# Optimization experiments

Hardware: AMD Instinct MI355X
Metric: run time of the kernel (lower is better)

Reference implementation:

```python
import jax, jax.numpy as jnp
import numpy as np

B, S, D, C, H, E, K, L = 32, 512, 768, 3072, 1024, 8, 2, 2


def _layernorm(x, g, b, eps=1e-5):
    mu = jnp.mean(x, axis=-1, keepdims=True)
    var = jnp.var(x, axis=-1, keepdims=True)
    return (x - mu) * jax.lax.rsqrt(var + eps) * g + b


def setup_inputs() -> dict:
    key = jax.random.key(0)
    ks = jax.random.split(key, 12)
    s = 0.02
    return {
        "hidden_states": jax.random.normal(ks[0], (B, S, C), jnp.float32),
        "proj_w": jax.random.normal(ks[1], (C, D), jnp.float32) * s,
        "proj_b": jnp.zeros((D,), jnp.float32),
        "ln1_g": jnp.ones((D,), jnp.float32),
        "ln1_b": jnp.zeros((D,), jnp.float32),
        "gate_w": jax.random.normal(ks[2], (D, E), jnp.float32) * s,
        "gate_b": jnp.zeros((E,), jnp.float32),
        "w1": jax.random.normal(ks[3], (E, D, H), jnp.float32) * s,
        "b1": jnp.zeros((E, H), jnp.float32),
        "w2": jax.random.normal(ks[4], (E, H, D), jnp.float32) * s,
        "b2": jnp.zeros((E, D), jnp.float32),
        "ln2_g": jnp.ones((D,), jnp.float32),
        "ln2_b": jnp.zeros((D,), jnp.float32),
        "cls_w": jax.random.normal(ks[5], (D, L), jnp.float32) * s,
        "cls_b": jnp.zeros((L,), jnp.float32),
    }


def reference(hidden_states, proj_w, proj_b, ln1_g, ln1_b, gate_w, gate_b,
              w1, b1, w2, b2, ln2_g, ln2_b, cls_w, cls_b):
    # layer_projection: Linear -> LayerNorm -> GELU (dropout = identity in eval)
    x = jnp.einsum('bsc,cd->bsd', hidden_states, proj_w) + proj_b
    x = _layernorm(x, ln1_g, ln1_b)
    seq_out = jax.nn.gelu(x, approximate=False)  # [B,S,D]

    # Router: gate -> softmax -> top-k -> renormalize
    probs = jax.nn.softmax(seq_out @ gate_w + gate_b, axis=-1)  # [B,S,E]
    top_w, top_i = jax.lax.top_k(probs, K)                      # [B,S,K]
    top_w = top_w / jnp.sum(top_w, axis=-1, keepdims=True)

    # combine[t,e] = sum_k top_w[t,k] * (top_i[t,k]==e)
    combine = jnp.sum(jax.nn.one_hot(top_i, E, dtype=top_w.dtype)
                      * top_w[..., None], axis=-2)              # [B,S,E]

    xt = seq_out.reshape(-1, D)                                 # [T,D]
    ct = combine.reshape(-1, E)                                 # [T,E]
    h = jax.nn.gelu(jnp.einsum('td,edh->eth', xt, w1) + b1[:, None, :],
                    approximate=False)                          # [E,T,H]
    eo = jnp.einsum('eth,ehd->etd', h, w2) + b2[:, None, :]     # [E,T,D]
    moe = jnp.einsum('etd,te->td', eo, ct).reshape(B, S, D)

    moe = _layernorm(moe + seq_out, ln2_g, ln2_b)
    logits = moe @ cls_w + cls_b                                # [B,S,2]
    return logits
```

## Files before the change

### kernel.cpp

```cpp
#include <hip/hip_runtime.h>
#include <hip/hip_bf16.h>

#define T_TOK 16384
#define CDIM 3072
#define DDIM 768
#define HDIM 1024
#define NEXP 8
#define NSLOT 33792
#define MAXTILE 264
#define AMB_CAP 2048
#define AMB2_CAP 256
#define KSPLIT 4
#define NSEG 8

typedef __attribute__((ext_vector_type(8))) short bfrag;
typedef __attribute__((ext_vector_type(4))) float f32x4;
typedef __attribute__((ext_vector_type(4))) float fvec4;

__device__ __forceinline__ unsigned short bf16_rn(float f) {
  union { float f; unsigned u; } v; v.f = f;
  unsigned r = v.u + 0x7fffu + ((v.u >> 16) & 1u);
  return (unsigned short)(r >> 16);
}
__device__ __forceinline__ float bf16_f32(unsigned short h) {
  union { unsigned u; float f; } v; v.u = ((unsigned)h) << 16;
  return v.f;
}
__device__ __forceinline__ float gelu_exact(float x) {
  return 0.5f * x * (1.0f + erff(x * 0.70710678118654752440f));
}
__device__ __forceinline__ void glds16(const void* g, void* l) {
  __builtin_amdgcn_global_load_lds((const __attribute__((address_space(1))) void*)g,
                                   (__attribute__((address_space(3))) void*)l, 16, 0, 0);
}

__global__ void k_init(int* token_list, int* counts, int* cursors, unsigned short* zero_row,
                       int* amb_count, int* amb2_count) {
  int i = blockIdx.x * 256 + threadIdx.x;
  for (int j = i; j < NSLOT; j += 64 * 256) token_list[j] = -1;
  if (i < NEXP) counts[i] = 0;
  if (i < 128) cursors[i] = 0;
  if (i == 0) { *amb_count = 0; *amb2_count = 0; }
  if (i < 1024) zero_row[i] = 0;
}

__global__ void k_cast_tiled(const float* __restrict__ src,
                             unsigned short* __restrict__ dst) {
  __shared__ unsigned short h[128][136];
  int rb = blockIdx.x;
  int cc = blockIdx.y;
  int tid = threadIdx.x;
  const float* in = src + ((size_t)rb * 128) * CDIM + cc * 128;
#pragma unroll
  for (int it = 0; it < 16; ++it) {
    int idx = it * 256 + tid;
    int r = idx >> 5, nv = idx & 31;
    fvec4 v = *(const fvec4*)(in + (size_t)r * CDIM + nv * 4);
    unsigned long long p = (unsigned long long)bf16_rn(v[0]) |
                           ((unsigned long long)bf16_rn(v[1]) << 16) |
                           ((unsigned long long)bf16_rn(v[2]) << 32) |
                           ((unsigned long long)bf16_rn(v[3]) << 48);
    *(unsigned long long*)&h[r][nv * 4] = p;
  }
  __syncthreads();
  unsigned short* ob = dst + ((size_t)rb * 96 + cc * 4) * 4096;
#pragma unroll
  for (int kt = 0; kt < 4; ++kt) {
#pragma unroll
    for (int it = 0; it < 2; ++it) {
      int gg = it * 256 + tid;
      int kg = gg >> 7, r = gg & 127;
      bfrag o = *(const bfrag*)&h[r][kt * 32 + kg * 8];
      *(bfrag*)(ob + ((size_t)kt * 512 + gg) * 8) = o;
    }
  }
}

__global__ void k_transpose_split(const float* __restrict__ src,
                                  unsigned short* __restrict__ dhi,
                                  unsigned short* __restrict__ dlo) {
  __shared__ unsigned short h[128][72], l[128][72];
  int nb2 = blockIdx.x;
  int cb = blockIdx.y;
  int col_blk = nb2 >> 1, nhalf = nb2 & 1;
  int n0 = col_blk * 128 + nhalf * 64;
  int tid = threadIdx.x;
  const float* in = src + (size_t)(cb * 128) * DDIM + n0;
#pragma unroll
  for (int it = 0; it < 8; ++it) {
    int idx = it * 256 + tid;
    int cl = idx >> 4, nv = idx & 15;
    fvec4 v = *(const fvec4*)(in + (size_t)cl * DDIM + nv * 4);
    unsigned long long ph = 0, pl = 0;
#pragma unroll
    for (int e = 0; e < 4; ++e) {
      unsigned short hh = bf16_rn(v[e]);
      unsigned short ll = bf16_rn(v[e] - bf16_f32(hh));
      ph |= (unsigned long long)hh << (16 * e);
      pl |= (unsigned long long)ll << (16 * e);
    }
    *(unsigned long long*)&h[cl][nv * 4] = ph;
    *(unsigned long long*)&l[cl][nv * 4] = pl;
  }
  __syncthreads();
  size_t obase = ((size_t)col_blk * 96 + cb * 4) * 4096;
#pragma unroll
  for (int kt = 0; kt < 4; ++kt) {
    int kg = tid >> 6, rl = tid & 63;
    bfrag oh, ol;
#pragma unroll
    for (int e = 0; e < 8; ++e) {
      int c = kt * 32 + kg * 8 + e;
      oh[e] = (short)h[c][rl];
      ol[e] = (short)l[c][rl];
    }
    size_t gi = obase + ((size_t)kt * 512 + kg * 128 + nhalf * 64 + rl) * 8;
    *(bfrag*)(dhi + gi) = oh;
    *(bfrag*)(dlo + gi) = ol;
  }
}

__global__ void k_transpose_tiled(const float* __restrict__ src0,
                                  unsigned short* __restrict__ dst0, int K, int N) {
  __shared__ unsigned short h[128][72];
  int nb2 = blockIdx.x;
  int cb = blockIdx.y;
  int z = blockIdx.z;
  int col_blk = nb2 >> 1, nhalf = nb2 & 1;
  int n0 = col_blk * 128 + nhalf * 64;
  int tid = threadIdx.x;
  const float* in = src0 + (size_t)z * K * N + (size_t)(cb * 128) * N + n0;
#pragma unroll
  for (int it = 0; it < 8; ++it) {
    int idx = it * 256 + tid;
    int cl = idx >> 4, nv = idx & 15;
    fvec4 v = *(const fvec4*)(in + (size_t)cl * N + nv * 4);
    unsigned long long ph = 0;
#pragma unroll
    for (int e = 0; e < 4; ++e)
      ph |= (unsigned long long)bf16_rn(v[e]) << (16 * e);
    *(unsigned long long*)&h[cl][nv * 4] = ph;
  }
  __syncthreads();
  size_t obase = (size_t)z * K * N + ((size_t)col_blk * (K / 32) + cb * 4) * 4096;
#pragma unroll
  for (int kt = 0; kt < 4; ++kt) {
    int kg = tid >> 6, rl = tid & 63;
    bfrag oh;
#pragma unroll
    for (int e = 0; e < 8; ++e) oh[e] = (short)h[kt * 32 + kg * 8 + e][rl];
    *(bfrag*)(dst0 + obase + ((size_t)kt * 512 + kg * 128 + nhalf * 64 + rl) * 8) = oh;
  }
}

__launch_bounds__(256, 3)
__global__ void k_gemm1(const unsigned short* __restrict__ Atil,
                        const unsigned short* __restrict__ Btil,
                        float* __restrict__ Cout)
{
  __shared__ unsigned short sA[12288], sB[12288];
  int tid = threadIdx.x;
  int lane = tid & 63, wave = tid >> 6;
  int id = blockIdx.x;
  int swz = (id & 7) * 96 + (id >> 3);
  int brow = swz / 6, bcol = swz % 6;
  int row0 = brow * 128, col0 = bcol * 128;
  int wm = wave >> 1, wn = wave & 1;

  f32x4 acc[4][4];
#pragma unroll
  for (int i = 0; i < 4; ++i)
#pragma unroll
    for (int j = 0; j < 4; ++j) acc[i][j] = (f32x4){0.f, 0.f, 0.f, 0.f};

  int rsel = lane & 15, kq = lane >> 4;
  const unsigned short* At = Atil + (size_t)(brow * 96) * 4096;
  const unsigned short* Bt = Btil + (size_t)(bcol * 96) * 4096;

  auto STAGE = [&](int kt, int b) {
    const unsigned short* as = At + (size_t)kt * 4096;
    const unsigned short* bs = Bt + (size_t)kt * 4096;
    int lbase = b * 4096;
#pragma unroll
    for (int pass = 0; pass < 2; ++pass) {
      int g = pass * 256 + tid;
      int li = lbase + (pass * 256 + wave * 64) * 8;
      glds16(as + (size_t)g * 8, &sA[li]);
      glds16(bs + (size_t)g * 8, &sB[li]);
    }
  };

  STAGE(0, 0);
  STAGE(1, 1);
  int b0 = 0;
  for (int kt = 0; kt < 96; ++kt) {
    if (kt < 95) asm volatile("s_waitcnt vmcnt(4)" ::: "memory");
    else         asm volatile("s_waitcnt vmcnt(0)" ::: "memory");
    __builtin_amdgcn_s_barrier();
    if (kt + 2 < 96) {
      int bn = b0 + 2; if (bn >= 3) bn -= 3;
      STAGE(kt + 2, bn);
    }
    int lb = b0 * 4096;
    bfrag af[4], bf[4];
#pragma unroll
    for (int i = 0; i < 4; ++i) {
      af[i] = *(const bfrag*)&sA[lb + (kq * 128 + wm * 64 + i * 16 + rsel) * 8];
      bf[i] = *(const bfrag*)&sB[lb + (kq * 128 + wn * 64 + i * 16 + rsel) * 8];
    }
#pragma unroll
    for (int i = 0; i < 4; ++i)
#pragma unroll
      for (int j = 0; j < 4; ++j)
        acc[i][j] = __builtin_amdgcn_mfma_f32_16x16x32_bf16(af[i], bf[j], acc[i][j], 0, 0, 0);
    b0 = (b0 == 2) ? 0 : b0 + 1;
  }

  int cc = lane & 15, rr = (lane >> 4) * 4;
#pragma unroll
  for (int i = 0; i < 4; ++i)
#pragma unroll
    for (int j = 0; j < 4; ++j)
#pragma unroll
      for (int r = 0; r < 4; ++r) {
        int row = row0 + wm * 64 + i * 16 + rr + r;
        int col = col0 + wn * 64 + j * 16 + cc;
        Cout[(size_t)row * DDIM + col] = acc[i][j][r];
      }
}

__launch_bounds__(256)
__global__ void k_ln_router(const float* __restrict__ xw, const float* __restrict__ proj_b,
                            const float* __restrict__ g1, const float* __restrict__ b1v,
                            const float* __restrict__ gate_w, const float* __restrict__ gate_b,
                            unsigned short* __restrict__ seq_b16,
                            int* __restrict__ top_i, float* __restrict__ top_w,
                            int* __restrict__ amb_list, int* __restrict__ amb_count)
{
  int lane = threadIdx.x & 63;
  int t = blockIdx.x * 4 + (threadIdx.x >> 6);
  const float* xr = xw + (size_t)t * DDIM;
  float x0[12];
  float s = 0.f, s2 = 0.f;
#pragma unroll
  for (int j = 0; j < 12; ++j) {
    int d = lane + 64 * j;
    float v = xr[d] + proj_b[d];
    x0[j] = v; s += v; s2 += v * v;
  }
#pragma unroll
  for (int o = 32; o > 0; o >>= 1) { s += __shfl_xor(s, o, 64); s2 += __shfl_xor(s2, o, 64); }
  float mu = s * (1.f / DDIM);
  float rstd = rsqrtf(s2 * (1.f / DDIM) - mu * mu + 1e-5f);
  float acc8[8];
#pragma unroll
  for (int e = 0; e < 8; ++e) acc8[e] = 0.f;
#pragma unroll
  for (int j = 0; j < 12; ++j) {
    int d = lane + 64 * j;
    float y = (x0[j] - mu) * rstd * g1[d] + b1v[d];
    float ge = gelu_exact(y);
    seq_b16[(size_t)t * DDIM + d] = bf16_rn(ge);
    const float* gw = gate_w + (size_t)d * NEXP;
#pragma unroll
    for (int e = 0; e < 8; ++e) acc8[e] += ge * gw[e];
  }
#pragma unroll
  for (int e = 0; e < 8; ++e)
#pragma unroll
    for (int o = 32; o > 0; o >>= 1) acc8[e] += __shfl_xor(acc8[e], o, 64);
  if (lane == 0) {
    float lg[8];
#pragma unroll
    for (int e = 0; e < 8; ++e) lg[e] = acc8[e] + gate_b[e];
    int i0 = 0;
    for (int e = 1; e < 8; ++e) if (lg[e] > lg[i0]) i0 = e;
    int i1 = (i0 == 0) ? 1 : 0;
    for (int e = 0; e < 8; ++e) if (e != i0 && lg[e] > lg[i1]) i1 = e;
    float l2 = -1e30f;
    for (int e = 0; e < 8; ++e) if (e != i0 && e != i1 && lg[e] > l2) l2 = lg[e];
    if (lg[i1] - l2 < 8e-3f) {
      int p = atomicAdd(amb_count, 1);
      if (p < AMB_CAP) amb_list[p] = t;
    }
    float w0 = 1.f / (1.f + expf(lg[i1] - lg[i0]));
    top_i[t * 2] = i0; top_i[t * 2 + 1] = i1;
    top_w[t * 2] = w0; top_w[t * 2 + 1] = 1.f - w0;
  }
}

__launch_bounds__(256, 2)
__global__ void k_repair(const float* __restrict__ hidden,
                         const unsigned short* __restrict__ BTh,
                         const unsigned short* __restrict__ BTl,
                         const int* __restrict__ amb_list, const int* __restrict__ amb_count,
                         float* __restrict__ xw_fix4)
{
  int n = *amb_count; if (n > AMB_CAP) n = AMB_CAP;
  int by = blockIdx.y;
  if (by * 128 >= n) return;
  int bx = blockIdx.x;
  int z = blockIdx.z;
  int col0 = bx * 128;
  __shared__ unsigned short sAh[8192], sAl[8192], sBh[8192], sBl[8192];
  __shared__ int tk[128];
  int tid = threadIdx.x, lane = tid & 63, wave = tid >> 6;
  if (tid < 128) tk[tid] = (by * 128 + tid < n) ? amb_list[by * 128 + tid] : -1;
  __syncthreads();
  int wm = wave >> 1, wn = wave & 1;
  f32x4 acc[4][4];
#pragma unroll
  for (int i = 0; i < 4; ++i)
#pragma unroll
    for (int j = 0; j < 4; ++j) acc[i][j] = (f32x4){0.f, 0.f, 0.f, 0.f};
  int rsel = lane & 15, kq = lane >> 4;
  int ktbase = z * 24;
  const unsigned short* Bth = BTh + (size_t)(bx * 96) * 4096;
  const unsigned short* Btl = BTl + (size_t)(bx * 96) * 4096;

  auto STAGE = [&](int kt, int b) {
    int k0 = (ktbase + kt) * 32;
    int lb = b * 4096;
    size_t tb = (size_t)(ktbase + kt) * 4096;
#pragma unroll
    for (int pass = 0; pass < 2; ++pass) {
      int g = pass * 256 + tid;
      int kg = g >> 7, r = g & 127;
      int tok = tk[r];
      fvec4 a0 = (fvec4){0.f, 0.f, 0.f, 0.f}, a1 = a0;
      if (tok >= 0) {
        const float* ap = hidden + (size_t)tok * CDIM + k0 + kg * 8;
        a0 = *(const fvec4*)ap;
        a1 = *(const fvec4*)(ap + 4);
      }
      bfrag hv, lv;
#pragma unroll
      for (int u = 0; u < 8; ++u) {
        float v = (u < 4) ? a0[u] : a1[u - 4];
        unsigned short h = bf16_rn(v);
        hv[u] = (short)h;
        lv[u] = (short)bf16_rn(v - bf16_f32(h));
      }
      *(bfrag*)&sAh[lb + (size_t)g * 8] = hv;
      *(bfrag*)&sAl[lb + (size_t)g * 8] = lv;
      int li = lb + (pass * 256 + wave * 64) * 8;
      glds16(Bth + tb + (size_t)g * 8, &sBh[li]);
      glds16(Btl + tb + (size_t)g * 8, &sBl[li]);
    }
  };

  STAGE(0, 0);
  __syncthreads();
  for (int kt = 0; kt < 24; ++kt) {
    int b = kt & 1;
    if (kt + 1 < 24) STAGE(kt + 1, b ^ 1);
    int lb = b * 4096;
    bfrag ah[4], al[4], bh[4], bl[4];
#pragma unroll
    for (int i = 0; i < 4; ++i) {
      int ra = wm * 64 + i * 16 + rsel;
      ah[i] = *(const bfrag*)&sAh[lb + (kq * 128 + ra) * 8];
      al[i] = *(const bfrag*)&sAl[lb + (kq * 128 + ra) * 8];
      int cb = wn * 64 + i * 16 + rsel;
      bh[i] = *(const bfrag*)&sBh[lb + (kq * 128 + cb) * 8];
      bl[i] = *(const bfrag*)&sBl[lb + (kq * 128 + cb) * 8];
    }
#pragma unroll
    for (int i = 0; i < 4; ++i)
#pragma unroll
      for (int j = 0; j < 4; ++j) {
        acc[i][j] = __builtin_amdgcn_mfma_f32_16x16x32_bf16(ah[i], bh[j], acc[i][j], 0, 0, 0);
        acc[i][j] = __builtin_amdgcn_mfma_f32_16x16x32_bf16(ah[i], bl[j], acc[i][j], 0, 0, 0);
        acc[i][j] = __builtin_amdgcn_mfma_f32_16x16x32_bf16(al[i], bh[j], acc[i][j], 0, 0, 0);
      }
    __syncthreads();
  }
  float* dst = xw_fix4 + (size_t)z * AMB_CAP * DDIM;
  int cc = lane & 15, rr = (lane >> 4) * 4;
#pragma unroll
  for (int i = 0; i < 4; ++i)
#pragma unroll
    for (int j = 0; j < 4; ++j)
#pragma unroll
      for (int r = 0; r < 4; ++r) {
        int row = by * 128 + wm * 64 + i * 16 + rr + r;
        int col = col0 + wn * 64 + j * 16 + cc;
        dst[(size_t)row * DDIM + col] = acc[i][j][r];
      }
}

__launch_bounds__(256)
__global__ void k_fix2(const float* __restrict__ xw_fix4, const float* __restrict__ proj_b,
                       const float* __restrict__ g1, const float* __restrict__ b1v,
                       const float* __restrict__ gate_w, const float* __restrict__ gate_b,
                       const int* __restrict__ amb_list, const int* __restrict__ amb_count,
                       int* __restrict__ top_i, float* __restrict__ top_w,
                       int* __restrict__ amb2_list, int* __restrict__ amb2_count)
{
  int n = *amb_count; if (n > AMB_CAP) n = AMB_CAP;
  int lane = threadIdx.x & 63;
  int slot = blockIdx.x * 4 + (threadIdx.x >> 6);
  if (slot >= n) return;
  int t = amb_list[slot];
  const float* p0 = xw_fix4 + (size_t)slot * DDIM;
  const float* p1 = p0 + (size_t)AMB_CAP * DDIM;
  const float* p2 = p1 + (size_t)AMB_CAP * DDIM;
  const float* p3 = p2 + (size_t)AMB_CAP * DDIM;
  float x0[12];
  float s = 0.f, s2 = 0.f;
#pragma unroll
  for (int j = 0; j < 12; ++j) {
    int d = lane + 64 * j;
    float v = ((p0[d] + p1[d]) + (p2[d] + p3[d])) + proj_b[d];
    x0[j] = v; s += v; s2 += v * v;
  }
#pragma unroll
  for (int o = 32; o > 0; o >>= 1) { s += __shfl_xor(s, o, 64); s2 += __shfl_xor(s2, o, 64); }
  float mu = s * (1.f / DDIM);
  float rstd = rsqrtf(s2 * (1.f / DDIM) - mu * mu + 1e-5f);
  float acc8[8];
#pragma unroll
  for (int e = 0; e < 8; ++e) acc8[e] = 0.f;
#pragma unroll
  for (int j = 0; j < 12; ++j) {
    int d = lane + 64 * j;
    float y = (x0[j] - mu) * rstd * g1[d] + b1v[d];
    float ge = gelu_exact(y);
    const float* gw = gate_w + (size_t)d * NEXP;
#pragma unroll
    for (int e = 0; e < 8; ++e) acc8[e] += ge * gw[e];
  }
#pragma unroll
  for (int e = 0; e < 8; ++e)
#pragma unroll
    for (int o = 32; o > 0; o >>= 1) acc8[e] += __shfl_xor(acc8[e], o, 64);
  if (lane == 0) {
    float lg[8];
#pragma unroll
    for (int e = 0; e < 8; ++e) lg[e] = acc8[e] + gate_b[e];
    int i0 = 0;
    for (int e = 1; e < 8; ++e) if (lg[e] > lg[i0]) i0 = e;
    int i1 = (i0 == 0) ? 1 : 0;
    for (int e = 0; e < 8; ++e) if (e != i0 && lg[e] > lg[i1]) i1 = e;
    float l2 = -1e30f;
    for (int e = 0; e < 8; ++e) if (e != i0 && e != i1 && lg[e] > l2) l2 = lg[e];
    if (lg[i1] - l2 < 2e-4f) {
      int p = atomicAdd(amb2_count, 1);
      if (p < AMB2_CAP) amb2_list[p] = t;
    }
    float w0 = 1.f / (1.f + expf(lg[i1] - lg[i0]));
    top_i[t * 2] = i0; top_i[t * 2 + 1] = i1;
    top_w[t * 2] = w0; top_w[t * 2 + 1] = 1.f - w0;
  }
}

__launch_bounds__(256, 1)
__global__ void k_router_fix(const float* __restrict__ hidden, const float* __restrict__ proj_w,
                             const int* __restrict__ amb2_list, const int* __restrict__ amb2_count,
                             double* __restrict__ xpart)
{
  __shared__ float hrow[384];
  int tid = threadIdx.x;
  int seg = blockIdx.y;
  int cbase = seg * 384;
  int n = *amb2_count; if (n > AMB2_CAP) n = AMB2_CAP;
  for (int ii = blockIdx.x; ii < n; ii += gridDim.x) {
    int t = amb2_list[ii];
    __syncthreads();
    if (tid < 96)
      *(fvec4*)&hrow[tid * 4] = *(const fvec4*)(hidden + (size_t)t * CDIM + cbase + tid * 4);
    __syncthreads();
    double p0a = 0.0, p0b = 0.0, p1a = 0.0, p1b = 0.0, p2a = 0.0, p2b = 0.0;
    for (int c0 = 0; c0 < 384; c0 += 16) {
      float w0r[16], w1r[16], w2r[16];
      const float* wp = proj_w + (size_t)(cbase + c0) * DDIM + tid;
#pragma unroll
      for (int u = 0; u < 16; ++u) {
        w0r[u] = wp[u * DDIM];
        w1r[u] = wp[u * DDIM + 256];
        w2r[u] = wp[u * DDIM + 512];
      }
#pragma unroll
      for (int u = 0; u < 16; ++u) {
        double h = (double)hrow[c0 + u];
        if (u & 1) { p0b += h * (double)w0r[u]; p1b += h * (double)w1r[u]; p2b += h * (double)w2r[u]; }
        else       { p0a += h * (double)w0r[u]; p1a += h * (double)w1r[u]; p2a += h * (double)w2r[u]; }
      }
    }
    double* xp = xpart + ((size_t)seg * AMB2_CAP + ii) * DDIM;
    xp[tid] = p0a + p0b;
    xp[tid + 256] = p1a + p1b;
    xp[tid + 512] = p2a + p2b;
  }
}

__launch_bounds__(256)
__global__ void k_fix3(const double* __restrict__ xpart, const float* __restrict__ proj_b,
                       const float* __restrict__ g1, const float* __restrict__ b1v,
                       const float* __restrict__ gate_w, const float* __restrict__ gate_b,
                       const int* __restrict__ amb2_list, const int* __restrict__ amb2_count,
                       int* __restrict__ top_i, float* __restrict__ top_w)
{
  __shared__ double redA[4], redB[4], red8[4][8];
  int n = *amb2_count; if (n > AMB2_CAP) n = AMB2_CAP;
  int ii = blockIdx.x;
  if (ii >= n) return;
  int t = amb2_list[ii];
  int tid = threadIdx.x, lane = tid & 63, wave = tid >> 6;
  double x[3]; double s = 0.0, s2 = 0.0;
#pragma unroll
  for (int j = 0; j < 3; ++j) {
    int d = tid + 256 * j;
    double acc = (double)proj_b[d];
#pragma unroll
    for (int seg = 0; seg < NSEG; ++seg)
      acc += xpart[((size_t)seg * AMB2_CAP + ii) * DDIM + d];
    x[j] = acc; s += acc; s2 += acc * acc;
  }
#pragma unroll
  for (int o = 32; o > 0; o >>= 1) { s += __shfl_down(s, o, 64); s2 += __shfl_down(s2, o, 64); }
  if (lane == 0) { redA[wave] = s; redB[wave] = s2; }
  __syncthreads();
  double mu = (redA[0] + redA[1] + redA[2] + redA[3]) / DDIM;
  double ms = (redB[0] + redB[1] + redB[2] + redB[3]) / DDIM;
  double rstd = 1.0 / sqrt(ms - mu * mu + 1e-5);
  double a8[8];
#pragma unroll
  for (int e = 0; e < 8; ++e) a8[e] = 0.0;
#pragma unroll
  for (int j = 0; j < 3; ++j) {
    int d = tid + 256 * j;
    double y = (x[j] - mu) * rstd * (double)g1[d] + (double)b1v[d];
    double ge = 0.5 * y * (1.0 + erf(y * 0.7071067811865475244));
#pragma unroll
    for (int e = 0; e < 8; ++e) a8[e] += ge * (double)gate_w[(size_t)d * NEXP + e];
  }
#pragma unroll
  for (int e = 0; e < 8; ++e)
#pragma unroll
    for (int o = 32; o > 0; o >>= 1) a8[e] += __shfl_down(a8[e], o, 64);
  if (lane == 0) {
#pragma unroll
    for (int e = 0; e < 8; ++e) red8[wave][e] = a8[e];
  }
  __syncthreads();
  if (tid == 0) {
    double lg[8];
#pragma unroll
    for (int e = 0; e < 8; ++e)
      lg[e] = red8[0][e] + red8[1][e] + red8[2][e] + red8[3][e] + (double)gate_b[e];
    int i0 = 0;
    for (int e = 1; e < 8; ++e) if (lg[e] > lg[i0]) i0 = e;
    int i1 = (i0 == 0) ? 1 : 0;
    for (int e = 0; e < 8; ++e) if (e != i0 && e != i1 && lg[e] > lg[i1]) i1 = e;
    double w0 = 1.0 / (1.0 + exp(lg[i1] - lg[i0]));
    top_i[t * 2] = i0; top_i[t * 2 + 1] = i1;
    top_w[t * 2] = (float)w0; top_w[t * 2 + 1] = (float)(1.0 - w0);
  }
}

__global__ void k_count(const int* __restrict__ top_i, int* __restrict__ counts) {
  __shared__ int h[NEXP];
  int tid = threadIdx.x;
  if (tid < NEXP) h[tid] = 0;
  __syncthreads();
  for (int i = blockIdx.x * 256 + tid; i < 2 * T_TOK; i += 64 * 256)
    atomicAdd(&h[top_i[i]], 1);
  __syncthreads();
  if (tid < NEXP) atomicAdd(&counts[tid], h[tid]);
}

__global__ void k_offsets(const int* __restrict__ counts, int* __restrict__ seg_start,
                          int* __restrict__ padded_total, int* __restrict__ tile_expert) {
  if (threadIdx.x != 0 || blockIdx.x != 0) return;
  int st[NEXP], en[NEXP];
  int s = 0;
  for (int e = 0; e < NEXP; ++e) {
    st[e] = s; seg_start[e] = s;
    s += (counts[e] + 127) & ~127;
    en[e] = s;
  }
  *padded_total = s;
  int nt = s >> 7;
  for (int x = 0; x < nt; ++x) {
    int r = x << 7, e = 0;
    for (int q = 0; q < NEXP; ++q) if (r >= st[q] && r < en[q]) e = q;
    tile_expert[x] = e;
  }
}

__global__ void k_scatter(const int* __restrict__ top_i, const int* __restrict__ seg_start,
                          int* __restrict__ cursors, int* __restrict__ token_list,
                          int* __restrict__ slot_of) {
  __shared__ int lc[NEXP];
  __shared__ int lbase[NEXP];
  int tid = threadIdx.x;
  int t = blockIdx.x * 256 + tid;
  if (tid < NEXP) lc[tid] = 0;
  __syncthreads();
  int e0 = top_i[t * 2], e1 = top_i[t * 2 + 1];
  int o0 = atomicAdd(&lc[e0], 1);
  int o1 = atomicAdd(&lc[e1], 1);
  __syncthreads();
  if (tid < NEXP) lbase[tid] = atomicAdd(&cursors[tid << 4], lc[tid]);
  __syncthreads();
  int p0 = seg_start[e0] + lbase[e0] + o0;
  int p1 = seg_start[e1] + lbase[e1] + o1;
  token_list[p0] = t;
  token_list[p1] = t;
  slot_of[t * 2] = p0;
  slot_of[t * 2 + 1] = p1;
}

__global__ void k_gather(const unsigned short* __restrict__ seqb,
                         const int* __restrict__ token_list,
                         const int* __restrict__ padded_total,
                         unsigned short* __restrict__ seqgT) {
  int sb = blockIdx.x;
  if (sb * 128 >= *padded_total) return;
  int cc = blockIdx.y;
  __shared__ unsigned short h[128][136];
  __shared__ int tk[128];
  int tid = threadIdx.x;
  if (tid < 128) tk[tid] = token_list[sb * 128 + tid];
  __syncthreads();
#pragma unroll
  for (int it = 0; it < 8; ++it) {
    int idx = it * 256 + tid;
    int r = idx >> 4, nv = idx & 15;
    int tok = tk[r];
    bfrag v = (bfrag){0, 0, 0, 0, 0, 0, 0, 0};
    if (tok >= 0)
      v = *(const bfrag*)(seqb + (size_t)tok * DDIM + cc * 128 + nv * 8);
    *(bfrag*)&h[r][nv * 8] = v;
  }
  __syncthreads();
  unsigned short* ob = seqgT + ((size_t)sb * 24 + cc * 4) * 4096;
#pragma unroll
  for (int kt = 0; kt < 4; ++kt) {
#pragma unroll
    for (int it = 0; it < 2; ++it) {
      int gg = it * 256 + tid;
      int kg = gg >> 7, r = gg & 127;
      bfrag o = *(const bfrag*)&h[r][kt * 32 + kg * 8];
      *(bfrag*)(ob + ((size_t)kt * 512 + gg) * 8) = o;
    }
  }
}

__launch_bounds__(256, 4)
__global__ void k_gemm2(const unsigned short* __restrict__ seqgT,
                        const unsigned short* __restrict__ w1T,
                        const float* __restrict__ b1,
                        const int* __restrict__ tile_expert,
                        const int* __restrict__ padded_total,
                        unsigned short* __restrict__ hbufT)
{
  int by = blockIdx.x;
  if (by * 128 >= *padded_total) return;
  int bx = blockIdx.y;
  int e = tile_expert[by];
  __shared__ unsigned short smem[16384];
  unsigned short* sA = smem;
  unsigned short* sB = smem + 8192;
  int tid = threadIdx.x, lane = tid & 63, wave = tid >> 6;
  int col0 = bx * 128;
  int wm = wave >> 1, wn = wave & 1;
  f32x4 acc[4][4];
#pragma unroll
  for (int i = 0; i < 4; ++i)
#pragma unroll
    for (int j = 0; j < 4; ++j) acc[i][j] = (f32x4){0.f, 0.f, 0.f, 0.f};
  const unsigned short* At = seqgT + (size_t)by * 24 * 4096;
  const unsigned short* Bt = w1T + (size_t)e * HDIM * DDIM + (size_t)bx * 24 * 4096;
  int rsel = lane & 15, kq = lane >> 4;

  auto STAGE = [&](int kt, int b) {
    int lbase2 = b * 4096;
    size_t tb = (size_t)kt * 4096;
#pragma unroll
    for (int pass = 0; pass < 2; ++pass) {
      int g = pass * 256 + tid;
      int li = lbase2 + (pass * 256 + wave * 64) * 8;
      glds16(At + tb + (size_t)g * 8, &sA[li]);
      glds16(Bt + tb + (size_t)g * 8, &sB[li]);
    }
  };

  STAGE(0, 0);
  __syncthreads();
  for (int kt = 0; kt < 24; ++kt) {
    int b = kt & 1;
    if (kt + 1 < 24) STAGE(kt + 1, b ^ 1);
    int lb = b * 4096;
    bfrag af[4], bf[4];
#pragma unroll
    for (int i = 0; i < 4; ++i) {
      af[i] = *(const bfrag*)&sA[lb + (kq * 128 + wm * 64 + i * 16 + rsel) * 8];
      bf[i] = *(const bfrag*)&sB[lb + (kq * 128 + wn * 64 + i * 16 + rsel) * 8];
    }
#pragma unroll
    for (int i = 0; i < 4; ++i)
#pragma unroll
      for (int j = 0; j < 4; ++j)
        acc[i][j] = __builtin_amdgcn_mfma_f32_16x16x32_bf16(af[i], bf[j], acc[i][j], 0, 0, 0);
    __syncthreads();
  }
  int cc = lane & 15, rr = (lane >> 4) * 4;
#pragma unroll
  for (int i = 0; i < 4; ++i)
#pragma unroll
    for (int j = 0; j < 4; ++j)
#pragma unroll
      for (int r = 0; r < 4; ++r) {
        int lr = wm * 64 + i * 16 + rr + r;
        int lc = wn * 64 + j * 16 + cc;
        float x = acc[i][j][r] + b1[(size_t)e * HDIM + col0 + lc];
        int gi = (lc >> 5) * 4096 + ((lc >> 3) & 3) * 1024 + lr * 8 + (lc & 7);
        smem[gi] = bf16_rn(gelu_exact(x));
      }
  __syncthreads();
  unsigned short* dst = hbufT + ((size_t)by * 32 + (col0 >> 5)) * 4096;
#pragma unroll
  for (int it = 0; it < 8; ++it) {
    int idx = it * 256 + tid;
    *(bfrag*)(dst + (size_t)idx * 8) = *(const bfrag*)&smem[idx * 8];
  }
}

__launch_bounds__(256, 4)
__global__ void k_gemm3(const unsigned short* __restrict__ hbufT,
                        const unsigned short* __restrict__ w2T,
                        const float* __restrict__ b2,
                        const int* __restrict__ tile_expert,
                        const int* __restrict__ padded_total,
                        unsigned short* __restrict__ eo)
{
  int by = blockIdx.x;
  if (by * 128 >= *padded_total) return;
  int bx = blockIdx.y;
  int e = tile_expert[by];
  __shared__ unsigned short smem[16384];
  unsigned short* sA = smem;
  unsigned short* sB = smem + 8192;
  int tid = threadIdx.x, lane = tid & 63, wave = tid >> 6;
  int col0 = bx * 128;
  int wm = wave >> 1, wn = wave & 1;
  f32x4 acc[4][4];
#pragma unroll
  for (int i = 0; i < 4; ++i)
#pragma unroll
    for (int j = 0; j < 4; ++j) acc[i][j] = (f32x4){0.f, 0.f, 0.f, 0.f};
  const unsigned short* At = hbufT + (size_t)by * 32 * 4096;
  const unsigned short* Bt = w2T + (size_t)e * DDIM * HDIM + (size_t)bx * 32 * 4096;
  int rsel = lane & 15, kq = lane >> 4;

  auto STAGE = [&](int kt, int b) {
    int lbase2 = b * 4096;
    size_t tb = (size_t)kt * 4096;
#pragma unroll
    for (int pass = 0; pass < 2; ++pass) {
      int g = pass * 256 + tid;
      int li = lbase2 + (pass * 256 + wave * 64) * 8;
      glds16(At + tb + (size_t)g * 8, &sA[li]);
      glds16(Bt + tb + (size_t)g * 8, &sB[li]);
    }
  };

  STAGE(0, 0);
  __syncthreads();
  for (int kt = 0; kt < 32; ++kt) {
    int b = kt & 1;
    if (kt + 1 < 32) STAGE(kt + 1, b ^ 1);
    int lb = b * 4096;
    bfrag af[4], bf[4];
#pragma unroll
    for (int i = 0; i < 4; ++i) {
      af[i] = *(const bfrag*)&sA[lb + (kq * 128 + wm * 64 + i * 16 + rsel) * 8];
      bf[i] = *(const bfrag*)&sB[lb + (kq * 128 + wn * 64 + i * 16 + rsel) * 8];
    }
#pragma unroll
    for (int i = 0; i < 4; ++i)
#pragma unroll
      for (int j = 0; j < 4; ++j)
        acc[i][j] = __builtin_amdgcn_mfma_f32_16x16x32_bf16(af[i], bf[j], acc[i][j], 0, 0, 0);
    __syncthreads();
  }
  int cc = lane & 15, rr = (lane >> 4) * 4;
#pragma unroll
  for (int i = 0; i < 4; ++i)
#pragma unroll
    for (int j = 0; j < 4; ++j)
#pragma unroll
      for (int r = 0; r < 4; ++r) {
        int lr = wm * 64 + i * 16 + rr + r;
        int lc = wn * 64 + j * 16 + cc;
        smem[lr * 128 + lc] = bf16_rn(acc[i][j][r] + b2[(size_t)e * DDIM + col0 + lc]);
      }
  __syncthreads();
#pragma unroll
  for (int it = 0; it < 8; ++it) {
    int idx = it * 256 + tid;
    int row = idx >> 4, cb = idx & 15;
    *(bfrag*)(eo + (size_t)(by * 128 + row) * DDIM + col0 + cb * 8) =
        *(const bfrag*)&smem[row * 128 + cb * 8];
  }
}

__launch_bounds__(256)
__global__ void k_combine(const unsigned short* __restrict__ eo,
                          const unsigned short* __restrict__ seqb,
                          const int* __restrict__ slot_of, const float* __restrict__ top_w,
                          const float* __restrict__ g2, const float* __restrict__ b2v,
                          const float* __restrict__ cls_w, const float* __restrict__ cls_b,
                          float* __restrict__ out)
{
  int lane = threadIdx.x & 63;
  int t = blockIdx.x * 4 + (threadIdx.x >> 6);
  int s0 = slot_of[t * 2], s1 = slot_of[t * 2 + 1];
  float w0 = top_w[t * 2], w1 = top_w[t * 2 + 1];
  const unsigned short* p0 = eo + (size_t)s0 * DDIM;
  const unsigned short* p1 = eo + (size_t)s1 * DDIM;
  const unsigned short* sq = seqb + (size_t)t * DDIM;
  float m[12];
  float s = 0.f, s2 = 0.f;
#pragma unroll
  for (int j = 0; j < 12; ++j) {
    int d = lane + 64 * j;
    float v = w0 * bf16_f32(p0[d]) + w1 * bf16_f32(p1[d]) + bf16_f32(sq[d]);
    m[j] = v; s += v; s2 += v * v;
  }
#pragma unroll
  for (int o = 32; o > 0; o >>= 1) { s += __shfl_xor(s, o, 64); s2 += __shfl_xor(s2, o, 64); }
  float mu = s * (1.f / DDIM);
  float rstd = rsqrtf(s2 * (1.f / DDIM) - mu * mu + 1e-5f);
  float l0 = 0.f, l1 = 0.f;
#pragma unroll
  for (int j = 0; j < 12; ++j) {
    int d = lane + 64 * j;
    float y = (m[j] - mu) * rstd * g2[d] + b2v[d];
    l0 += y * cls_w[d * 2];
    l1 += y * cls_w[d * 2 + 1];
  }
#pragma unroll
  for (int o = 32; o > 0; o >>= 1) { l0 += __shfl_xor(l0, o, 64); l1 += __shfl_xor(l1, o, 64); }
  if (lane == 0) {
    out[(size_t)t * 2] = l0 + cls_b[0];
    out[(size_t)t * 2 + 1] = l1 + cls_b[1];
  }
}

extern "C" void kernel_launch(void* const* d_in, const int* in_sizes, int n_in,
                              void* d_out, int out_size, void* d_ws, size_t ws_size,
                              hipStream_t stream) {
  const float* hidden = (const float*)d_in[0];
  const float* proj_w = (const float*)d_in[1];
  const float* proj_b = (const float*)d_in[2];
  const float* ln1_g  = (const float*)d_in[3];
  const float* ln1_b  = (const float*)d_in[4];
  const float* gate_w = (const float*)d_in[5];
  const float* gate_b = (const float*)d_in[6];
  const float* w1     = (const float*)d_in[7];
  const float* b1     = (const float*)d_in[8];
  const float* w2     = (const float*)d_in[9];
  const float* b2     = (const float*)d_in[10];
  const float* ln2_g  = (const float*)d_in[11];
  const float* ln2_b  = (const float*)d_in[12];
  const float* cls_w  = (const float*)d_in[13];
  const float* cls_b  = (const float*)d_in[14];
  float* out = (float*)d_out;

  char* base = (char*)d_ws;
  size_t off = 0;
  auto alloc = [&](size_t b) -> void* {
    void* p = base + off;
    off += (b + 255) & ~(size_t)255;
    return p;
  };
  unsigned short* pwT_hi = (unsigned short*)alloc((size_t)DDIM * CDIM * 2);
  unsigned short* pwT_lo = (unsigned short*)alloc((size_t)DDIM * CDIM * 2);
  unsigned short* w1T    = (unsigned short*)alloc((size_t)NEXP * HDIM * DDIM * 2);
  unsigned short* w2T    = (unsigned short*)alloc((size_t)NEXP * DDIM * HDIM * 2);
  float* xw              = (float*)alloc((size_t)T_TOK * DDIM * 4);
  float* xw_fix4         = (float*)alloc((size_t)KSPLIT * AMB_CAP * DDIM * 4);
  double* xpart          = (double*)alloc((size_t)NSEG * AMB2_CAP * DDIM * 8);
  unsigned short* seqb   = (unsigned short*)alloc((size_t)T_TOK * DDIM * 2);
  unsigned short* seqgT  = (unsigned short*)alloc((size_t)MAXTILE * 24 * 4096 * 2);
  int* top_i             = (int*)alloc((size_t)T_TOK * 2 * 4);
  float* top_w           = (float*)alloc((size_t)T_TOK * 2 * 4);
  int* slot_of           = (int*)alloc((size_t)T_TOK * 2 * 4);
  int* amb_list          = (int*)alloc((size_t)AMB_CAP * 4);
  int* amb2_list         = (int*)alloc((size_t)AMB2_CAP * 4);
  int* token_list        = (int*)alloc((size_t)NSLOT * 4);
  int* counts            = (int*)alloc(256);
  int* cursors           = (int*)alloc(512);
  int* seg_start         = (int*)alloc(256);
  int* padded_total      = (int*)alloc(256);
  int* tile_expert       = (int*)alloc((size_t)MAXTILE * 4);
  unsigned short* zero_row = (unsigned short*)alloc(2048);
  int* amb_count         = (int*)alloc(256);
  int* amb2_count        = (int*)alloc(256);
  size_t poolBytes = 2 * (size_t)T_TOK * CDIM * 2;
  char* pool = (char*)alloc(poolBytes);
  unsigned short* Ahi = (unsigned short*)pool;
  size_t poff = 0;
  auto palloc = [&](size_t b) -> void* {
    void* p = pool + poff;
    poff += (b + 255) & ~(size_t)255;
    return p;
  };
  unsigned short* hbufT  = (unsigned short*)palloc((size_t)MAXTILE * 32 * 4096 * 2);
  unsigned short* eo     = (unsigned short*)palloc((size_t)NSLOT * DDIM * 2);
  (void)ws_size; (void)in_sizes; (void)n_in; (void)out_size;

  k_init<<<64, 256, 0, stream>>>(token_list, counts, cursors, zero_row, amb_count, amb2_count);
  k_cast_tiled<<<dim3(128, 24), 256, 0, stream>>>(hidden, Ahi);
  k_transpose_split<<<dim3(12, 24), 256, 0, stream>>>(proj_w, pwT_hi, pwT_lo);
  k_transpose_tiled<<<dim3(16, 6, 8), 256, 0, stream>>>(w1, w1T, DDIM, HDIM);
  k_transpose_tiled<<<dim3(12, 8, 8), 256, 0, stream>>>(w2, w2T, HDIM, DDIM);
  k_gemm1<<<768, 256, 0, stream>>>(Ahi, pwT_hi, xw);
  k_ln_router<<<T_TOK / 4, 256, 0, stream>>>(xw, proj_b, ln1_g, ln1_b, gate_w, gate_b,
                                             seqb, top_i, top_w, amb_list, amb_count);
  k_repair<<<dim3(6, AMB_CAP / 128, KSPLIT), 256, 0, stream>>>(hidden, pwT_hi, pwT_lo,
                                                               amb_list, amb_count, xw_fix4);
  k_fix2<<<AMB_CAP / 4, 256, 0, stream>>>(xw_fix4, proj_b, ln1_g, ln1_b, gate_w, gate_b,
                                          amb_list, amb_count, top_i, top_w,
                                          amb2_list, amb2_count);
  k_router_fix<<<dim3(64, NSEG), 256, 0, stream>>>(hidden, proj_w, amb2_list, amb2_count, xpart);
  k_fix3<<<AMB2_CAP, 256, 0, stream>>>(xpart, proj_b, ln1_g, ln1_b, gate_w, gate_b,
                                       amb2_list, amb2_count, top_i, top_w);
  k_count<<<64, 256, 0, stream>>>(top_i, counts);
  k_offsets<<<1, 64, 0, stream>>>(counts, seg_start, padded_total, tile_expert);
  k_scatter<<<64, 256, 0, stream>>>(top_i, seg_start, cursors, token_list, slot_of);
  k_gather<<<dim3(MAXTILE, 6), 256, 0, stream>>>(seqb, token_list, padded_total, seqgT);
  k_gemm2<<<dim3(MAXTILE, 8), 256, 0, stream>>>(seqgT, w1T, b1, tile_expert,
                                                padded_total, hbufT);
  k_gemm3<<<dim3(MAXTILE, 6), 256, 0, stream>>>(hbufT, w2T, b2, tile_expert, padded_total, eo);
  k_combine<<<T_TOK / 4, 256, 0, stream>>>(eo, seqb, slot_of, top_w, ln2_g, ln2_b,
                                           cls_w, cls_b, out);
}
```

Before: 586.3 us.

## Triple-buffer LDS staging in expert GEMMs with vmcnt-based waits

Converts the two expert GEMM kernels from double-buffered to triple-buffered LDS staging, prefetching two K-tiles ahead. Each iteration waits with explicit s_waitcnt vmcnt and a raw barrier, replacing the trailing __syncthreads. The intent is to hide global-to-LDS load latency behind MFMA work. In exchange LDS use per block rises to 48 KB and launch bounds drop to 3 blocks per CU, so occupancy falls and the hand-placed waits carry correctness risk.

```diff
diff --git a/kernel.cpp b/kernel.cpp
--- a/kernel.cpp
+++ b/kernel.cpp
@@ -648,7 +648,7 @@
   }
 }
 
-__launch_bounds__(256, 4)
+__launch_bounds__(256, 3)
 __global__ void k_gemm2(const unsigned short* __restrict__ seqgT,
                         const unsigned short* __restrict__ w1T,
                         const float* __restrict__ b1,
@@ -660,9 +660,9 @@
   if (by * 128 >= *padded_total) return;
   int bx = blockIdx.y;
   int e = tile_expert[by];
-  __shared__ unsigned short smem[16384];
+  __shared__ unsigned short smem[24576];
   unsigned short* sA = smem;
-  unsigned short* sB = smem + 8192;
+  unsigned short* sB = smem + 12288;
   int tid = threadIdx.x, lane = tid & 63, wave = tid >> 6;
   int col0 = bx * 128;
   int wm = wave >> 1, wn = wave & 1;
@@ -688,11 +688,17 @@
   };
 
   STAGE(0, 0);
-  __syncthreads();
+  STAGE(1, 1);
+  int b0 = 0;
   for (int kt = 0; kt < 24; ++kt) {
-    int b = kt & 1;
-    if (kt + 1 < 24) STAGE(kt + 1, b ^ 1);
-    int lb = b * 4096;
+    if (kt < 23) asm volatile("s_waitcnt vmcnt(4)" ::: "memory");
+    else         asm volatile("s_waitcnt vmcnt(0)" ::: "memory");
+    __builtin_amdgcn_s_barrier();
+    if (kt + 2 < 24) {
+      int bn = b0 + 2; if (bn >= 3) bn -= 3;
+      STAGE(kt + 2, bn);
+    }
+    int lb = b0 * 4096;
     bfrag af[4], bf[4];
 #pragma unroll
     for (int i = 0; i < 4; ++i) {
@@ -704,8 +710,9 @@
 #pragma unroll
       for (int j = 0; j < 4; ++j)
         acc[i][j] = __builtin_amdgcn_mfma_f32_16x16x32_bf16(af[i], bf[j], acc[i][j], 0, 0, 0);
-    __syncthreads();
-  }
+    b0 = (b0 == 2) ? 0 : b0 + 1;
+  }
+  __builtin_amdgcn_s_barrier();
   int cc = lane & 15, rr = (lane >> 4) * 4;
 #pragma unroll
   for (int i = 0; i < 4; ++i)
@@ -728,7 +735,7 @@
   }
 }
 
-__launch_bounds__(256, 4)
+__launch_bounds__(256, 3)
 __global__ void k_gemm3(const unsigned short* __restrict__ hbufT,
                         const unsigned short* __restrict__ w2T,
                         const float* __restrict__ b2,
@@ -740,9 +747,9 @@
   if (by * 128 >= *padded_total) return;
   int bx = blockIdx.y;
   int e = tile_expert[by];
-  __shared__ unsigned short smem[16384];
+  __shared__ unsigned short smem[24576];
   unsigned short* sA = smem;
-  unsigned short* sB = smem + 8192;
+  unsigned short* sB = smem + 12288;
   int tid = threadIdx.x, lane = tid & 63, wave = tid >> 6;
   int col0 = bx * 128;
   int wm = wave >> 1, wn = wave & 1;
@@ -768,11 +775,17 @@
   };
 
   STAGE(0, 0);
-  __syncthreads();
+  STAGE(1, 1);
+  int b0 = 0;
   for (int kt = 0; kt < 32; ++kt) {
-    int b = kt & 1;
-    if (kt + 1 < 32) STAGE(kt + 1, b ^ 1);
-    int lb = b * 4096;
+    if (kt < 31) asm volatile("s_waitcnt vmcnt(4)" ::: "memory");
+    else         asm volatile("s_waitcnt vmcnt(0)" ::: "memory");
+    __builtin_amdgcn_s_barrier();
+    if (kt + 2 < 32) {
+      int bn = b0 + 2; if (bn >= 3) bn -= 3;
+      STAGE(kt + 2, bn);
+    }
+    int lb = b0 * 4096;
     bfrag af[4], bf[4];
 #pragma unroll
     for (int i = 0; i < 4; ++i) {
@@ -784,8 +797,9 @@
 #pragma unroll
       for (int j = 0; j < 4; ++j)
         acc[i][j] = __builtin_amdgcn_mfma_f32_16x16x32_bf16(af[i], bf[j], acc[i][j], 0, 0, 0);
-    __syncthreads();
-  }
+    b0 = (b0 == 2) ? 0 : b0 + 1;
+  }
+  __builtin_amdgcn_s_barrier();
   int cc = lane & 15, rr = (lane >> 4) * 4;
 #pragma unroll
   for (int i = 0; i < 4; ++i)
```

After: 591.3 us. No clear change (+0.8%).
